# Performance work log

Hardware: AMD Instinct MI355X
Metric: run time of the kernel (lower is better)

## Reference

```python
import jax, jax.numpy as jnp
import numpy as np

DIM = 512
HEADS = 16
WS = (2, 7, 7)
N = WS[0] * WS[1] * WS[2]  # 98
NW = 64  # number of windows in mask
B_ = 512  # num_windows * batch
HEAD_DIM = DIM // HEADS
SCALE = HEAD_DIM ** -0.5
TABLE = (2 * WS[0] - 1) * (2 * WS[1] - 1) * (2 * WS[2] - 1)  # 507


def _relative_position_index():
    # Faithful to the repo (note: middle coord is NOT multiplied by (2*Ww-1),
    # matching the source exactly).
    ct, ch, cw = np.arange(WS[0]), np.arange(WS[1]), np.arange(WS[2])
    coords = np.stack(np.meshgrid(ct, ch, cw, indexing='ij'))  # [3,Th,Tw,Tw]
    flat = coords.reshape(3, -1)  # [3,N]
    rel = flat[:, :, None] - flat[:, None, :]  # [3,N,N]
    rel = rel.transpose(1, 2, 0).copy()  # [N,N,3]
    rel[:, :, 0] += WS[0] - 1
    rel[:, :, 1] += WS[1] - 1
    rel[:, :, 2] += WS[2] - 1
    rel[:, :, 0] *= (2 * WS[1] - 1) * (2 * WS[2] - 1)
    return rel.sum(-1).astype(np.int32)  # [N,N]


def setup_inputs() -> dict:
    key = jax.random.key(0)
    ks = jax.random.split(key, 7)
    x = jax.random.normal(ks[0], (B_, N, DIM), dtype=jnp.float32)
    mask = jnp.zeros((NW, N, N), dtype=jnp.float32)
    qkv_w = jax.random.normal(ks[1], (3 * DIM, DIM), dtype=jnp.float32) * (DIM ** -0.5)
    qkv_b = jnp.zeros((3 * DIM,), dtype=jnp.float32)
    proj_w = jax.random.normal(ks[2], (DIM, DIM), dtype=jnp.float32) * (DIM ** -0.5)
    proj_b = jnp.zeros((DIM,), dtype=jnp.float32)
    bias_table = jax.random.normal(ks[3], (TABLE, HEADS), dtype=jnp.float32) * 0.02
    rel_index = jnp.asarray(_relative_position_index())
    return {"x": x, "mask": mask, "qkv_w": qkv_w, "qkv_b": qkv_b,
            "proj_w": proj_w, "proj_b": proj_b, "bias_table": bias_table,
            "rel_index": rel_index}


def reference(x, mask, qkv_w, qkv_b, proj_w, proj_b, bias_table, rel_index):
    Bw, n, c = x.shape
    # QKV projection -> [3, B_, H, N, hd]
    qkv = (x @ qkv_w.T + qkv_b).reshape(Bw, n, 3, HEADS, HEAD_DIM)
    qkv = qkv.transpose(2, 0, 3, 1, 4)
    q, k, v = qkv[0], qkv[1], qkv[2]
    attn = jnp.einsum('bhnd,bhmd->bhnm', q * SCALE, k)  # [B_,H,N,N]
    # Gathered relative position bias -> [H,N,N]
    bias = bias_table[rel_index.reshape(-1)].reshape(n, n, HEADS).transpose(2, 0, 1)
    attn = attn + bias[None]
    # Broadcast mask over batch groups of nW windows
    nW = mask.shape[0]
    attn = attn.reshape(Bw // nW, nW, HEADS, n, n) + mask[None, :, None]
    attn = attn.reshape(Bw, HEADS, n, n)
    attn = jax.nn.softmax(attn, axis=-1)
    out = jnp.einsum('bhnm,bhmd->bhnd', attn, v)
    out = out.transpose(0, 2, 1, 3).reshape(Bw, n, c)
    return out @ proj_w.T + proj_b
```

## Files before the change

### kernel.cpp

```cpp
#include <hip/hip_runtime.h>
#include <stdint.h>

#define HEADS 16
#define NTOK 98
#define HD 32
#define SCALE_Q 0.17677669529663687f

typedef __attribute__((ext_vector_type(4))) float floatx4;
typedef __attribute__((ext_vector_type(8))) short shortx8;

__device__ __forceinline__ unsigned short f2bf(float f) {
  union { float f; unsigned u; } v; v.f = f;
  unsigned r = v.u + 0x7fffu + ((v.u >> 16) & 1u);
  return (unsigned short)(r >> 16);
}
__device__ __forceinline__ float bf2f(unsigned short s) {
  union { unsigned u; float f; } v; v.u = ((unsigned)s) << 16;
  return v.f;
}

__device__ __forceinline__ void gload_lds16(const void* g, void* l) {
  __builtin_amdgcn_global_load_lds(
      (const __attribute__((address_space(1))) unsigned int*)g,
      (__attribute__((address_space(3))) unsigned int*)l, 16, 0, 0);
}

__global__ void convert_x_kernel(const float* __restrict__ x,
                                 unsigned short* __restrict__ xbf) {
  int idx = blockIdx.x * 256 + threadIdx.x;
  const float4 f0 = *(const float4*)(x + (size_t)idx * 8);
  const float4 f1 = *(const float4*)(x + (size_t)idx * 8 + 4);
  union { ushort us[8]; uint4 u4; } pk;
  pk.us[0] = f2bf(f0.x); pk.us[1] = f2bf(f0.y);
  pk.us[2] = f2bf(f0.z); pk.us[3] = f2bf(f0.w);
  pk.us[4] = f2bf(f1.x); pk.us[5] = f2bf(f1.y);
  pk.us[6] = f2bf(f1.z); pk.us[7] = f2bf(f1.w);
  *(uint4*)(xbf + (size_t)idx * 8) = pk.u4;
}

__global__ void convert_w_kernel(const float* __restrict__ qkv_w,
                                 const float* __restrict__ proj_w,
                                 unsigned short* __restrict__ wq,
                                 unsigned short* __restrict__ wp) {
  int idx = blockIdx.x * 256 + threadIdx.x;
  if (idx < 1536 * 512) wq[idx] = f2bf(qkv_w[idx]);
  if (idx < 512 * 512) wp[idx] = f2bf(proj_w[idx]);
}

__global__ void bm_kernel(const float* __restrict__ table,
                          const int* __restrict__ rel,
                          const float* __restrict__ mask,
                          unsigned short* __restrict__ bm) {
  int ij = blockIdx.x * 256 + threadIdx.x;
  int wh = blockIdx.y;
  int w = wh >> 4, h = wh & 15;
  if (ij < NTOK * NTOK) {
    float v = table[rel[ij] * HEADS + h] + mask[w * (NTOK * NTOK) + ij];
    bm[(size_t)wh * (NTOK * NTOK) + ij] = f2bf(v);
  }
}

__global__ __launch_bounds__(512, 4)
void qkv_gemm_kernel(const unsigned short* __restrict__ xbf,
                     const unsigned short* __restrict__ wbf,
                     const float* __restrict__ qkv_b,
                     unsigned short* __restrict__ q_out,
                     unsigned short* __restrict__ k_out,
                     unsigned short* __restrict__ v_out) {
  __shared__ unsigned short As[2][128 * 32];
  __shared__ unsigned short Bs[2][256 * 32];
  const int tid = threadIdx.x;
  const int wave = tid >> 6, lane = tid & 63;
  const int m0 = blockIdx.x * 128, n0 = blockIdx.y * 256;
  const int wm = wave & 1, wn = wave >> 1;
  const int ln15 = lane & 15, qd = lane >> 4;
  const int bl_r = lane >> 2, bl_s = lane & 3;

  const int sg_st = bl_s ^ ((bl_r >> 1) & 3);
  const int swz_rd = (qd ^ ((ln15 >> 1) & 3)) * 8;

  const int a_row = wave * 16 + bl_r;
  const unsigned short* aG = xbf + (size_t)(m0 + a_row) * 512 + sg_st * 8;
  const int b_row0 = wave * 32 + bl_r;
  const unsigned short* bG0 = wbf + (size_t)(n0 + b_row0) * 512 + sg_st * 8;
  const unsigned short* bG1 = wbf + (size_t)(n0 + b_row0 + 16) * 512 + sg_st * 8;

  floatx4 acc[4][4] = {};

  gload_lds16((const void*)aG, (void*)&As[0][wave * 16 * 32]);
  gload_lds16((const void*)bG0, (void*)&Bs[0][wave * 32 * 32]);
  gload_lds16((const void*)bG1, (void*)&Bs[0][(wave * 32 + 16) * 32]);
  __syncthreads();

  int cur = 0;
#pragma unroll 2
  for (int k0 = 0; k0 < 512; k0 += 32) {
    if (k0 + 32 < 512) {
      int nx = cur ^ 1;
      gload_lds16((const void*)(aG + k0 + 32), (void*)&As[nx][wave * 16 * 32]);
      gload_lds16((const void*)(bG0 + k0 + 32), (void*)&Bs[nx][wave * 32 * 32]);
      gload_lds16((const void*)(bG1 + k0 + 32),
                  (void*)&Bs[nx][(wave * 32 + 16) * 32]);
    }
    shortx8 afrag[4], bfrag[4];
#pragma unroll
    for (int mt = 0; mt < 4; ++mt)
      afrag[mt] =
          *(const shortx8*)&As[cur][(wm * 64 + mt * 16 + ln15) * 32 + swz_rd];
#pragma unroll
    for (int nt = 0; nt < 4; ++nt)
      bfrag[nt] =
          *(const shortx8*)&Bs[cur][(wn * 64 + nt * 16 + ln15) * 32 + swz_rd];
#pragma unroll
    for (int mt = 0; mt < 4; ++mt)
#pragma unroll
      for (int nt = 0; nt < 4; ++nt)
        acc[mt][nt] = __builtin_amdgcn_mfma_f32_16x16x32_bf16(
            afrag[mt], bfrag[nt], acc[mt][nt], 0, 0, 0);
    __syncthreads();
    cur ^= 1;
  }

#pragma unroll
  for (int mt = 0; mt < 4; ++mt) {
#pragma unroll
    for (int r = 0; r < 4; ++r) {
      int grow = m0 + wm * 64 + mt * 16 + qd * 4 + r;
      unsigned b = (unsigned)grow / 98u;
      unsigned i = (unsigned)grow - b * 98u;
#pragma unroll
      for (int nt = 0; nt < 4; ++nt) {
        int col = n0 + wn * 64 + nt * 16 + ln15;
        float val = acc[mt][nt][r] + qkv_b[col];
        int which = col >> 9;
        int h = (col >> 5) & 15;
        int d = col & 31;
        size_t oidx = ((size_t)(b * 16 + h) * 98 + i) * 32 + d;
        if (which == 0)      q_out[oidx] = f2bf(val * SCALE_Q);
        else if (which == 1) k_out[oidx] = f2bf(val);
        else                 v_out[oidx] = f2bf(val);
      }
    }
  }
}

__global__ __launch_bounds__(256, 6)
void attn_kernel(const unsigned short* __restrict__ qg,
                 const unsigned short* __restrict__ kg,
                 const unsigned short* __restrict__ vg,
                 const unsigned short* __restrict__ bmg,
                 unsigned short* __restrict__ outg) {
  __shared__ unsigned short Vt[32 * 136];
  __shared__ unsigned short Ps[4][16 * 40];
  const int tid = threadIdx.x;
  const int bh = blockIdx.x;
  const int b = bh >> 4, h = bh & 15, w = b & 63;
  const size_t base = (size_t)bh * (NTOK * HD);
  const int wave = tid >> 6, lane = tid & 63;
  const int ln15 = lane & 15, qd = lane >> 4;
  const unsigned short* bmh = bmg + (size_t)(w * 16 + h) * (NTOK * NTOK);

  for (int idx = tid; idx < 544; idx += 256)
    ((uint4*)Vt)[idx] = make_uint4(0, 0, 0, 0);
  __syncthreads();
  for (int t = tid; t < 392; t += 256) {
    int i = t >> 2, seg = t & 3;
    union { uint4 u4; unsigned short us[8]; } u;
    u.u4 = *(const uint4*)(vg + base + i * 32 + seg * 8);
    int d0 = seg * 8;
#pragma unroll
    for (int e = 0; e < 8; ++e) Vt[(d0 + e) * 136 + i] = u.us[e];
  }
  __syncthreads();

  floatx4 oacc[2];
#pragma unroll
  for (int mslot = 0; mslot < 2; ++mslot) {
    int mt = wave + mslot * 4;
    if (mt >= 7) break;
    shortx8 af = *(const shortx8*)(qg + base + (mt * 16 + ln15) * 32 + qd * 8);
    float s[7][4];
    {
      floatx4 sacc[7];
#pragma unroll
      for (int nt = 0; nt < 7; ++nt) {
        shortx8 bf = *(const shortx8*)(kg + base + (nt * 16 + ln15) * 32 + qd * 8);
        floatx4 z = {};
        sacc[nt] = __builtin_amdgcn_mfma_f32_16x16x32_bf16(af, bf, z, 0, 0, 0);
      }
#pragma unroll
      for (int r = 0; r < 4; ++r) {
        int i = mt * 16 + qd * 4 + r;
        int ii = i < 97 ? i : 97;
#pragma unroll
        for (int nt = 0; nt < 7; ++nt) {
          int j = nt * 16 + ln15;
          int jj = j < 97 ? j : 97;
          float bmv = bf2f(bmh[ii * NTOK + jj]);
          s[nt][r] = (i < NTOK && j < NTOK) ? sacc[nt][r] + bmv : -1e30f;
        }
      }
    }
    float linv[4];
#pragma unroll
    for (int r = 0; r < 4; ++r) {
      float mx = s[0][r];
#pragma unroll
      for (int nt = 1; nt < 7; ++nt) mx = fmaxf(mx, s[nt][r]);
#pragma unroll
      for (int off = 1; off < 16; off <<= 1)
        mx = fmaxf(mx, __shfl_xor(mx, off, 64));
      float sum = 0.f;
#pragma unroll
      for (int nt = 0; nt < 7; ++nt) {
        float p = __expf(s[nt][r] - mx);
        s[nt][r] = p;
        sum += p;
      }
#pragma unroll
      for (int off = 1; off < 16; off <<= 1) sum += __shfl_xor(sum, off, 64);
      linv[r] = 1.0f / sum;
    }
    oacc[0] = (floatx4){};
    oacc[1] = (floatx4){};
#pragma unroll
    for (int ks = 0; ks < 4; ++ks) {
#pragma unroll
      for (int nt2 = 0; nt2 < 2; ++nt2) {
        int nt = ks * 2 + nt2;
#pragma unroll
        for (int r = 0; r < 4; ++r)
          Ps[wave][(qd * 4 + r) * 40 + nt2 * 16 + ln15] = f2bf(s[nt][r]);
      }
      shortx8 ap = *(const shortx8*)&Ps[wave][ln15 * 40 + qd * 8];
      shortx8 bv0 = *(const shortx8*)&Vt[ln15 * 136 + ks * 32 + qd * 8];
      shortx8 bv1 = *(const shortx8*)&Vt[(16 + ln15) * 136 + ks * 32 + qd * 8];
      oacc[0] = __builtin_amdgcn_mfma_f32_16x16x32_bf16(ap, bv0, oacc[0], 0, 0, 0);
      oacc[1] = __builtin_amdgcn_mfma_f32_16x16x32_bf16(ap, bv1, oacc[1], 0, 0, 0);
    }
#pragma unroll
    for (int r = 0; r < 4; ++r) {
      int i = mt * 16 + qd * 4 + r;
      if (i < NTOK) {
        size_t ob = ((size_t)b * NTOK + i) * 512 + h * 32;
#pragma unroll
        for (int vt = 0; vt < 2; ++vt)
          outg[ob + vt * 16 + ln15] = f2bf(oacc[vt][r] * linv[r]);
      }
    }
  }
}

__global__ __launch_bounds__(512, 4)
void proj_gemm_kernel(const unsigned short* __restrict__ a,
                      const unsigned short* __restrict__ wbf,
                      const float* __restrict__ proj_b,
                      float* __restrict__ out) {
  __shared__ unsigned short As[2][128 * 32];
  __shared__ unsigned short Bs[2][256 * 32];
  const int tid = threadIdx.x;
  const int wave = tid >> 6, lane = tid & 63;
  const int m0 = blockIdx.x * 128, n0 = blockIdx.y * 256;
  const int wm = wave & 1, wn = wave >> 1;
  const int ln15 = lane & 15, qd = lane >> 4;
  const int bl_r = lane >> 2, bl_s = lane & 3;

  const int sg_st = bl_s ^ ((bl_r >> 1) & 3);
  const int swz_rd = (qd ^ ((ln15 >> 1) & 3)) * 8;

  const int a_row = wave * 16 + bl_r;
  const unsigned short* aG = a + (size_t)(m0 + a_row) * 512 + sg_st * 8;
  const int b_row0 = wave * 32 + bl_r;
  const unsigned short* bG0 = wbf + (size_t)(n0 + b_row0) * 512 + sg_st * 8;
  const unsigned short* bG1 = wbf + (size_t)(n0 + b_row0 + 16) * 512 + sg_st * 8;

  floatx4 acc[4][4] = {};

  gload_lds16((const void*)aG, (void*)&As[0][wave * 16 * 32]);
  gload_lds16((const void*)bG0, (void*)&Bs[0][wave * 32 * 32]);
  gload_lds16((const void*)bG1, (void*)&Bs[0][(wave * 32 + 16) * 32]);
  __syncthreads();

  int cur = 0;
#pragma unroll 2
  for (int k0 = 0; k0 < 512; k0 += 32) {
    if (k0 + 32 < 512) {
      int nx = cur ^ 1;
      gload_lds16((const void*)(aG + k0 + 32), (void*)&As[nx][wave * 16 * 32]);
      gload_lds16((const void*)(bG0 + k0 + 32), (void*)&Bs[nx][wave * 32 * 32]);
      gload_lds16((const void*)(bG1 + k0 + 32),
                  (void*)&Bs[nx][(wave * 32 + 16) * 32]);
    }
    shortx8 afrag[4], bfrag[4];
#pragma unroll
    for (int mt = 0; mt < 4; ++mt)
      afrag[mt] =
          *(const shortx8*)&As[cur][(wm * 64 + mt * 16 + ln15) * 32 + swz_rd];
#pragma unroll
    for (int nt = 0; nt < 4; ++nt)
      bfrag[nt] =
          *(const shortx8*)&Bs[cur][(wn * 64 + nt * 16 + ln15) * 32 + swz_rd];
#pragma unroll
    for (int mt = 0; mt < 4; ++mt)
#pragma unroll
      for (int nt = 0; nt < 4; ++nt)
        acc[mt][nt] = __builtin_amdgcn_mfma_f32_16x16x32_bf16(
            afrag[mt], bfrag[nt], acc[mt][nt], 0, 0, 0);
    __syncthreads();
    cur ^= 1;
  }

#pragma unroll
  for (int mt = 0; mt < 4; ++mt) {
#pragma unroll
    for (int r = 0; r < 4; ++r) {
      int grow = m0 + wm * 64 + mt * 16 + qd * 4 + r;
#pragma unroll
      for (int nt = 0; nt < 4; ++nt) {
        int col = n0 + wn * 64 + nt * 16 + ln15;
        out[(size_t)grow * 512 + col] = acc[mt][nt][r] + proj_b[col];
      }
    }
  }
}

extern "C" void kernel_launch(void* const* d_in, const int* in_sizes, int n_in,
                              void* d_out, int out_size, void* d_ws, size_t ws_size,
                              hipStream_t stream) {
  const float* x          = (const float*)d_in[0];
  const float* mask       = (const float*)d_in[1];
  const float* qkv_w      = (const float*)d_in[2];
  const float* qkv_b      = (const float*)d_in[3];
  const float* proj_w     = (const float*)d_in[4];
  const float* proj_b     = (const float*)d_in[5];
  const float* bias_table = (const float*)d_in[6];
  const int*   rel_index  = (const int*)d_in[7];
  float* out = (float*)d_out;

  char* ws = (char*)d_ws;
  unsigned short* ws_qkvw  = (unsigned short*)(ws + 0);
  unsigned short* ws_projw = (unsigned short*)(ws + 1572864);
  unsigned short* ws_bm    = (unsigned short*)(ws + 2097152);
  unsigned short* ws_q     = (unsigned short*)(ws + 21766144);
  unsigned short* ws_k     = (unsigned short*)(ws + 73146368);
  unsigned short* ws_v     = (unsigned short*)(ws + 124526592);
  unsigned short* ws_attn  = (unsigned short*)(ws + 175906816);
  unsigned short* ws_xbf   = ws_attn;

  hipLaunchKernelGGL(convert_x_kernel, dim3(12544), dim3(256), 0, stream,
                     x, ws_xbf);
  hipLaunchKernelGGL(convert_w_kernel, dim3(3072), dim3(256), 0, stream,
                     qkv_w, proj_w, ws_qkvw, ws_projw);
  hipLaunchKernelGGL(bm_kernel, dim3(38, 1024), dim3(256), 0, stream,
                     bias_table, rel_index, mask, ws_bm);
  hipLaunchKernelGGL(qkv_gemm_kernel, dim3(392, 6), dim3(512), 0, stream,
                     ws_xbf, ws_qkvw, qkv_b, ws_q, ws_k, ws_v);
  hipLaunchKernelGGL(attn_kernel, dim3(8192), dim3(256), 0, stream,
                     ws_q, ws_k, ws_v, ws_bm, ws_attn);
  hipLaunchKernelGGL(proj_gemm_kernel, dim3(392, 2), dim3(512), 0, stream,
                     ws_attn, ws_projw, proj_b, out);
}
```

Baseline: 495.6 us.

## Pre-swizzle bias/mask into MFMA fragment layout and triple-buffer GEMM pipelines

Replaces the fused bf16 bias+mask table (one 98x98 entry per window and head, about 20 MB) with separate float bias (per head) and mask (per window) arrays. Both are laid out in MFMA accumulator fragment order, so the attention kernel reads them as contiguous floatx4 vectors and adds them, with padding handled through -1e30 entries instead of per-element branches. Both GEMMs move to a three-stage LDS pipeline with explicit vmcnt waits and one barrier per k-step, and their occupancy hint drops to 2. The V transpose store order is rotated per segment to cut LDS bank conflicts. The trade-offs are more LDS per block, lower occupancy hints, and float instead of bf16 reads for the bias data.

After: 523.6 us. 1.06x slower.

```diff
diff --git a/kernel.cpp b/kernel.cpp
--- a/kernel.cpp
+++ b/kernel.cpp
@@ -47,28 +47,48 @@
   if (idx < 512 * 512) wp[idx] = f2bf(proj_w[idx]);
 }
 
-__global__ void bm_kernel(const float* __restrict__ table,
-                          const int* __restrict__ rel,
-                          const float* __restrict__ mask,
-                          unsigned short* __restrict__ bm) {
-  int ij = blockIdx.x * 256 + threadIdx.x;
-  int wh = blockIdx.y;
-  int w = wh >> 4, h = wh & 15;
-  if (ij < NTOK * NTOK) {
-    float v = table[rel[ij] * HEADS + h] + mask[w * (NTOK * NTOK) + ij];
-    bm[(size_t)wh * (NTOK * NTOK) + ij] = f2bf(v);
-  }
-}
-
-__global__ __launch_bounds__(512, 4)
+__global__ void bmprep_kernel(const float* __restrict__ table,
+                              const int* __restrict__ rel,
+                              const float* __restrict__ mask,
+                              float* __restrict__ biasP,
+                              float* __restrict__ maskP) {
+  int idx = blockIdx.x * 256 + threadIdx.x;
+  if (idx < 229376) {
+    int e = idx & 31, lane = (idx >> 5) & 63;
+    int rest = idx >> 11;
+    int mt = rest % 7, h = rest / 7;
+    int nt = e >> 2, r = e & 3;
+    int i = mt * 16 + ((lane >> 4) << 2) + r;
+    int j = (nt << 4) + (lane & 15);
+    float v = 0.f;
+    if (nt < 7 && i < NTOK && j < NTOK) v = table[rel[i * NTOK + j] * HEADS + h];
+    biasP[idx] = v;
+  } else {
+    int t = idx - 229376;
+    int e = t & 31, lane = (t >> 5) & 63;
+    int rest = t >> 11;
+    int mt = rest % 7, wdx = rest / 7;
+    int nt = e >> 2, r = e & 3;
+    int i = mt * 16 + ((lane >> 4) << 2) + r;
+    int j = (nt << 4) + (lane & 15);
+    float v;
+    if (nt >= 7) v = 0.f;
+    else if (j >= NTOK) v = -1e30f;
+    else if (i >= NTOK) v = 0.f;
+    else v = mask[wdx * (NTOK * NTOK) + i * NTOK + j];
+    maskP[t] = v;
+  }
+}
+
+__global__ __launch_bounds__(512, 2)
 void qkv_gemm_kernel(const unsigned short* __restrict__ xbf,
                      const unsigned short* __restrict__ wbf,
                      const float* __restrict__ qkv_b,
                      unsigned short* __restrict__ q_out,
                      unsigned short* __restrict__ k_out,
                      unsigned short* __restrict__ v_out) {
-  __shared__ unsigned short As[2][128 * 32];
-  __shared__ unsigned short Bs[2][256 * 32];
+  __shared__ unsigned short As[3][128 * 32];
+  __shared__ unsigned short Bs[3][256 * 32];
   const int tid = threadIdx.x;
   const int wave = tid >> 6, lane = tid & 63;
   const int m0 = blockIdx.x * 128, n0 = blockIdx.y * 256;
@@ -79,47 +99,46 @@
   const int sg_st = bl_s ^ ((bl_r >> 1) & 3);
   const int swz_rd = (qd ^ ((ln15 >> 1) & 3)) * 8;
 
-  const int a_row = wave * 16 + bl_r;
-  const unsigned short* aG = xbf + (size_t)(m0 + a_row) * 512 + sg_st * 8;
-  const int b_row0 = wave * 32 + bl_r;
-  const unsigned short* bG0 = wbf + (size_t)(n0 + b_row0) * 512 + sg_st * 8;
-  const unsigned short* bG1 = wbf + (size_t)(n0 + b_row0 + 16) * 512 + sg_st * 8;
+  const unsigned short* aG = xbf + (size_t)(m0 + wave * 16 + bl_r) * 512 + sg_st * 8;
+  const unsigned short* bG0 = wbf + (size_t)(n0 + wave * 32 + bl_r) * 512 + sg_st * 8;
+  const unsigned short* bG1 = wbf + (size_t)(n0 + wave * 32 + 16 + bl_r) * 512 + sg_st * 8;
+
+#define QSTAGE(bufi, kk)                                                        \
+  do {                                                                          \
+    gload_lds16((const void*)(aG + (kk)), (void*)&As[bufi][wave * 512]);        \
+    gload_lds16((const void*)(bG0 + (kk)), (void*)&Bs[bufi][wave * 1024]);      \
+    gload_lds16((const void*)(bG1 + (kk)), (void*)&Bs[bufi][wave * 1024 + 512]);\
+  } while (0)
+
+  QSTAGE(0, 0);
+  QSTAGE(1, 32);
 
   floatx4 acc[4][4] = {};
-
-  gload_lds16((const void*)aG, (void*)&As[0][wave * 16 * 32]);
-  gload_lds16((const void*)bG0, (void*)&Bs[0][wave * 32 * 32]);
-  gload_lds16((const void*)bG1, (void*)&Bs[0][(wave * 32 + 16) * 32]);
-  __syncthreads();
-
-  int cur = 0;
-#pragma unroll 2
-  for (int k0 = 0; k0 < 512; k0 += 32) {
-    if (k0 + 32 < 512) {
-      int nx = cur ^ 1;
-      gload_lds16((const void*)(aG + k0 + 32), (void*)&As[nx][wave * 16 * 32]);
-      gload_lds16((const void*)(bG0 + k0 + 32), (void*)&Bs[nx][wave * 32 * 32]);
-      gload_lds16((const void*)(bG1 + k0 + 32),
-                  (void*)&Bs[nx][(wave * 32 + 16) * 32]);
-    }
+#pragma unroll
+  for (int it = 0; it < 16; ++it) {
+    if (it == 15) asm volatile("s_waitcnt vmcnt(0)" ::: "memory");
+    else          asm volatile("s_waitcnt vmcnt(3)" ::: "memory");
+    __builtin_amdgcn_sched_barrier(0);
+    __builtin_amdgcn_s_barrier();
+    __builtin_amdgcn_sched_barrier(0);
+    if (it + 2 < 16) QSTAGE((it + 2) % 3, (it + 2) * 32);
+    const unsigned short* Ab = As[it % 3];
+    const unsigned short* Bb = Bs[it % 3];
     shortx8 afrag[4], bfrag[4];
 #pragma unroll
     for (int mt = 0; mt < 4; ++mt)
-      afrag[mt] =
-          *(const shortx8*)&As[cur][(wm * 64 + mt * 16 + ln15) * 32 + swz_rd];
+      afrag[mt] = *(const shortx8*)&Ab[(wm * 64 + mt * 16 + ln15) * 32 + swz_rd];
 #pragma unroll
     for (int nt = 0; nt < 4; ++nt)
-      bfrag[nt] =
-          *(const shortx8*)&Bs[cur][(wn * 64 + nt * 16 + ln15) * 32 + swz_rd];
+      bfrag[nt] = *(const shortx8*)&Bb[(wn * 64 + nt * 16 + ln15) * 32 + swz_rd];
 #pragma unroll
     for (int mt = 0; mt < 4; ++mt)
 #pragma unroll
       for (int nt = 0; nt < 4; ++nt)
         acc[mt][nt] = __builtin_amdgcn_mfma_f32_16x16x32_bf16(
             afrag[mt], bfrag[nt], acc[mt][nt], 0, 0, 0);
-    __syncthreads();
-    cur ^= 1;
-  }
+  }
+#undef QSTAGE
 
 #pragma unroll
   for (int mt = 0; mt < 4; ++mt) {
@@ -144,11 +163,12 @@
   }
 }
 
-__global__ __launch_bounds__(256, 6)
+__global__ __launch_bounds__(256, 4)
 void attn_kernel(const unsigned short* __restrict__ qg,
                  const unsigned short* __restrict__ kg,
                  const unsigned short* __restrict__ vg,
-                 const unsigned short* __restrict__ bmg,
+                 const float* __restrict__ biasP,
+                 const float* __restrict__ maskP,
                  unsigned short* __restrict__ outg) {
   __shared__ unsigned short Vt[32 * 136];
   __shared__ unsigned short Ps[4][16 * 40];
@@ -158,7 +178,6 @@
   const size_t base = (size_t)bh * (NTOK * HD);
   const int wave = tid >> 6, lane = tid & 63;
   const int ln15 = lane & 15, qd = lane >> 4;
-  const unsigned short* bmh = bmg + (size_t)(w * 16 + h) * (NTOK * NTOK);
 
   for (int idx = tid; idx < 544; idx += 256)
     ((uint4*)Vt)[idx] = make_uint4(0, 0, 0, 0);
@@ -169,7 +188,10 @@
     u.u4 = *(const uint4*)(vg + base + i * 32 + seg * 8);
     int d0 = seg * 8;
 #pragma unroll
-    for (int e = 0; e < 8; ++e) Vt[(d0 + e) * 136 + i] = u.us[e];
+    for (int e0 = 0; e0 < 8; ++e0) {
+      int e = (e0 + seg * 2) & 7;
+      Vt[(d0 + e) * 136 + i] = u.us[e];
+    }
   }
   __syncthreads();
 
@@ -178,43 +200,37 @@
   for (int mslot = 0; mslot < 2; ++mslot) {
     int mt = wave + mslot * 4;
     if (mt >= 7) break;
+    const floatx4* bP = (const floatx4*)(biasP + (((size_t)h * 7 + mt) * 64 + lane) * 32);
+    const floatx4* mP = (const floatx4*)(maskP + (((size_t)w * 7 + mt) * 64 + lane) * 32);
+    floatx4 bb[7];
+#pragma unroll
+    for (int nt = 0; nt < 7; ++nt) bb[nt] = bP[nt] + mP[nt];
+
     shortx8 af = *(const shortx8*)(qg + base + (mt * 16 + ln15) * 32 + qd * 8);
-    float s[7][4];
-    {
-      floatx4 sacc[7];
-#pragma unroll
-      for (int nt = 0; nt < 7; ++nt) {
-        shortx8 bf = *(const shortx8*)(kg + base + (nt * 16 + ln15) * 32 + qd * 8);
-        floatx4 z = {};
-        sacc[nt] = __builtin_amdgcn_mfma_f32_16x16x32_bf16(af, bf, z, 0, 0, 0);
-      }
-#pragma unroll
-      for (int r = 0; r < 4; ++r) {
-        int i = mt * 16 + qd * 4 + r;
-        int ii = i < 97 ? i : 97;
-#pragma unroll
-        for (int nt = 0; nt < 7; ++nt) {
-          int j = nt * 16 + ln15;
-          int jj = j < 97 ? j : 97;
-          float bmv = bf2f(bmh[ii * NTOK + jj]);
-          s[nt][r] = (i < NTOK && j < NTOK) ? sacc[nt][r] + bmv : -1e30f;
-        }
-      }
-    }
+    floatx4 sacc[7];
+#pragma unroll
+    for (int nt = 0; nt < 7; ++nt) {
+      shortx8 bf = *(const shortx8*)(kg + base + (nt * 16 + ln15) * 32 + qd * 8);
+      floatx4 z = {};
+      sacc[nt] = __builtin_amdgcn_mfma_f32_16x16x32_bf16(af, bf, z, 0, 0, 0);
+    }
+#pragma unroll
+    for (int nt = 0; nt < 7; ++nt) sacc[nt] += bb[nt];
+
     float linv[4];
 #pragma unroll
     for (int r = 0; r < 4; ++r) {
-      float mx = s[0][r];
-#pragma unroll
-      for (int nt = 1; nt < 7; ++nt) mx = fmaxf(mx, s[nt][r]);
+      float mx = sacc[0][r];
+#pragma unroll
+      for (int nt = 1; nt < 7; ++nt) mx = fmaxf(mx, sacc[nt][r]);
 #pragma unroll
       for (int off = 1; off < 16; off <<= 1)
         mx = fmaxf(mx, __shfl_xor(mx, off, 64));
       float sum = 0.f;
 #pragma unroll
       for (int nt = 0; nt < 7; ++nt) {
-        float p = __expf(s[nt][r] - mx);
-        s[nt][r] = p;
+        float p = __expf(sacc[nt][r] - mx);
+        sacc[nt][r] = p;
         sum += p;
       }
 #pragma unroll
@@ -230,7 +246,7 @@
         int nt = ks * 2 + nt2;
 #pragma unroll
         for (int r = 0; r < 4; ++r)
-          Ps[wave][(qd * 4 + r) * 40 + nt2 * 16 + ln15] = f2bf(s[nt][r]);
+          Ps[wave][(qd * 4 + r) * 40 + nt2 * 16 + ln15] = f2bf(sacc[nt][r]);
       }
       shortx8 ap = *(const shortx8*)&Ps[wave][ln15 * 40 + qd * 8];
       shortx8 bv0 = *(const shortx8*)&Vt[ln15 * 136 + ks * 32 + qd * 8];
@@ -251,13 +267,13 @@
   }
 }
 
-__global__ __launch_bounds__(512, 4)
+__global__ __launch_bounds__(512, 2)
 void proj_gemm_kernel(const unsigned short* __restrict__ a,
                       const unsigned short* __restrict__ wbf,
                       const float* __restrict__ proj_b,
                       float* __restrict__ out) {
-  __shared__ unsigned short As[2][128 * 32];
-  __shared__ unsigned short Bs[2][256 * 32];
+  __shared__ unsigned short As[3][128 * 32];
+  __shared__ unsigned short Bs[3][256 * 32];
   const int tid = threadIdx.x;
   const int wave = tid >> 6, lane = tid & 63;
   const int m0 = blockIdx.x * 128, n0 = blockIdx.y * 256;
@@ -268,47 +284,46 @@
   const int sg_st = bl_s ^ ((bl_r >> 1) & 3);
   const int swz_rd = (qd ^ ((ln15 >> 1) & 3)) * 8;
 
-  const int a_row = wave * 16 + bl_r;
-  const unsigned short* aG = a + (size_t)(m0 + a_row) * 512 + sg_st * 8;
-  const int b_row0 = wave * 32 + bl_r;
-  const unsigned short* bG0 = wbf + (size_t)(n0 + b_row0) * 512 + sg_st * 8;
-  const unsigned short* bG1 = wbf + (size_t)(n0 + b_row0 + 16) * 512 + sg_st * 8;
+  const unsigned short* aG = a + (size_t)(m0 + wave * 16 + bl_r) * 512 + sg_st * 8;
+  const unsigned short* bG0 = wbf + (size_t)(n0 + wave * 32 + bl_r) * 512 + sg_st * 8;
+  const unsigned short* bG1 = wbf + (size_t)(n0 + wave * 32 + 16 + bl_r) * 512 + sg_st * 8;
+
+#define PSTAGE(bufi, kk)                                                        \
+  do {                                                                          \
+    gload_lds16((const void*)(aG + (kk)), (void*)&As[bufi][wave * 512]);        \
+    gload_lds16((const void*)(bG0 + (kk)), (void*)&Bs[bufi][wave * 1024]);      \
+    gload_lds16((const void*)(bG1 + (kk)), (void*)&Bs[bufi][wave * 1024 + 512]);\
+  } while (0)
+
+  PSTAGE(0, 0);
+  PSTAGE(1, 32);
 
   floatx4 acc[4][4] = {};
-
-  gload_lds16((const void*)aG, (void*)&As[0][wave * 16 * 32]);
-  gload_lds16((const void*)bG0, (void*)&Bs[0][wave * 32 * 32]);
-  gload_lds16((const void*)bG1, (void*)&Bs[0][(wave * 32 + 16) * 32]);
-  __syncthreads();
-
-  int cur = 0;
-#pragma unroll 2
-  for (int k0 = 0; k0 < 512; k0 += 32) {
-    if (k0 + 32 < 512) {
-      int nx = cur ^ 1;
-      gload_lds16((const void*)(aG + k0 + 32), (void*)&As[nx][wave * 16 * 32]);
-      gload_lds16((const void*)(bG0 + k0 + 32), (void*)&Bs[nx][wave * 32 * 32]);
-      gload_lds16((const void*)(bG1 + k0 + 32),
-                  (void*)&Bs[nx][(wave * 32 + 16) * 32]);
-    }
+#pragma unroll
+  for (int it = 0; it < 16; ++it) {
+    if (it == 15) asm volatile("s_waitcnt vmcnt(0)" ::: "memory");
+    else          asm volatile("s_waitcnt vmcnt(3)" ::: "memory");
+    __builtin_amdgcn_sched_barrier(0);
+    __builtin_amdgcn_s_barrier();
+    __builtin_amdgcn_sched_barrier(0);
+    if (it + 2 < 16) PSTAGE((it + 2) % 3, (it + 2) * 32);
+    const unsigned short* Ab = As[it % 3];
+    const unsigned short* Bb = Bs[it % 3];
     shortx8 afrag[4], bfrag[4];
 #pragma unroll
     for (int mt = 0; mt < 4; ++mt)
-      afrag[mt] =
-          *(const shortx8*)&As[cur][(wm * 64 + mt * 16 + ln15) * 32 + swz_rd];
+      afrag[mt] = *(const shortx8*)&Ab[(wm * 64 + mt * 16 + ln15) * 32 + swz_rd];
 #pragma unroll
     for (int nt = 0; nt < 4; ++nt)
-      bfrag[nt] =
-          *(const shortx8*)&Bs[cur][(wn * 64 + nt * 16 + ln15) * 32 + swz_rd];
+      bfrag[nt] = *(const shortx8*)&Bb[(wn * 64 + nt * 16 + ln15) * 32 + swz_rd];
 #pragma unroll
     for (int mt = 0; mt < 4; ++mt)
 #pragma unroll
       for (int nt = 0; nt < 4; ++nt)
         acc[mt][nt] = __builtin_amdgcn_mfma_f32_16x16x32_bf16(
             afrag[mt], bfrag[nt], acc[mt][nt], 0, 0, 0);
-    __syncthreads();
-    cur ^= 1;
-  }
+  }
+#undef PSTAGE
 
 #pragma unroll
   for (int mt = 0; mt < 4; ++mt) {
@@ -340,23 +355,24 @@
   char* ws = (char*)d_ws;
   unsigned short* ws_qkvw  = (unsigned short*)(ws + 0);
   unsigned short* ws_projw = (unsigned short*)(ws + 1572864);
-  unsigned short* ws_bm    = (unsigned short*)(ws + 2097152);
-  unsigned short* ws_q     = (unsigned short*)(ws + 21766144);
-  unsigned short* ws_k     = (unsigned short*)(ws + 73146368);
-  unsigned short* ws_v     = (unsigned short*)(ws + 124526592);
-  unsigned short* ws_attn  = (unsigned short*)(ws + 175906816);
+  float*          ws_biasP = (float*)(ws + 2097152);
+  float*          ws_maskP = (float*)(ws + 3014656);
+  unsigned short* ws_q     = (unsigned short*)(ws + 6684672);
+  unsigned short* ws_k     = (unsigned short*)(ws + 58064896);
+  unsigned short* ws_v     = (unsigned short*)(ws + 109445120);
+  unsigned short* ws_attn  = (unsigned short*)(ws + 160825344);
   unsigned short* ws_xbf   = ws_attn;
 
   hipLaunchKernelGGL(convert_x_kernel, dim3(12544), dim3(256), 0, stream,
                      x, ws_xbf);
   hipLaunchKernelGGL(convert_w_kernel, dim3(3072), dim3(256), 0, stream,
                      qkv_w, proj_w, ws_qkvw, ws_projw);
-  hipLaunchKernelGGL(bm_kernel, dim3(38, 1024), dim3(256), 0, stream,
-                     bias_table, rel_index, mask, ws_bm);
+  hipLaunchKernelGGL(bmprep_kernel, dim3(4480), dim3(256), 0, stream,
+                     bias_table, rel_index, mask, ws_biasP, ws_maskP);
   hipLaunchKernelGGL(qkv_gemm_kernel, dim3(392, 6), dim3(512), 0, stream,
                      ws_xbf, ws_qkvw, qkv_b, ws_q, ws_k, ws_v);
   hipLaunchKernelGGL(attn_kernel, dim3(8192), dim3(256), 0, stream,
-                     ws_q, ws_k, ws_v, ws_bm, ws_attn);
+                     ws_q, ws_k, ws_v, ws_biasP, ws_maskP, ws_attn);
   hipLaunchKernelGGL(proj_gemm_kernel, dim3(392, 2), dim3(512), 0, stream,
                      ws_attn, ws_projw, proj_b, out);
 }
```
